# Kernel tuning notes

Hardware: AMD Instinct MI355X
Metric: run time of the kernel (lower is better)

The kernel has to match this reference:

```python
import jax, jax.numpy as jnp
import numpy as np

EMB = 8
HID = 64
B = 1000
T = 512
N = (B * T) // 5  # events per source; sources partition the (batch,time) grid

_KEYS = ["ccba", "cdtx", "cust", "dp", "remit"]
_NUMS = {"ccba": 8, "cdtx": 1, "cust": 1, "dp": 2, "remit": 1}
_CATS = {"ccba": 0, "cdtx": 2, "cust": 3, "dp": 8, "remit": 1}
_VOCAB = {"ccba": 0, "cdtx": 179, "cust": 37, "dp": 435, "remit": 5}


def setup_inputs() -> dict:
    ks = iter(jax.random.split(jax.random.key(0), 64))
    rng = np.random.default_rng(0)
    chunks = np.split(rng.permutation(B * T), 5)
    d = {}
    for k5, ch in zip(_KEYS, chunks):
        d[k5 + "_num"] = jax.random.normal(next(ks), (N, _NUMS[k5]), jnp.float32)
        if _CATS[k5] > 0:
            d[k5 + "_cat"] = jax.random.randint(next(ks), (N, _CATS[k5]), 0, _VOCAB[k5])
            d[k5 + "_tab"] = jax.random.normal(next(ks), (_VOCAB[k5], EMB), jnp.float32) * 0.1
        d[k5 + "_bi"] = jnp.asarray(ch // T, jnp.int32)
        d[k5 + "_ti"] = jnp.asarray(ch % T, jnp.int32)
        in_dim = _CATS[k5] * EMB + _NUMS[k5]
        d[k5 + "_W"] = jax.random.normal(next(ks), (in_dim, HID), jnp.float32) * np.float32(1.0 / np.sqrt(in_dim))
        d[k5 + "_b"] = jnp.zeros((HID,), jnp.float32)
    # LSTM: 2 layers x 2 directions, hidden 64, proj_size 1 -> layer1 input is 2
    for l, insz in [(0, HID), (1, 2)]:
        d[f"Wih{l}"] = jax.random.normal(next(ks), (2, 4 * HID, insz), jnp.float32) * 0.05
        d[f"Whh{l}"] = jax.random.normal(next(ks), (2, 4 * HID, 1), jnp.float32) * 0.05
        d[f"Whr{l}"] = jax.random.normal(next(ks), (2, 1, HID), jnp.float32) * 0.05
        d[f"bih{l}"] = jnp.zeros((2, 4 * HID), jnp.float32)
        d[f"bhh{l}"] = jnp.zeros((2, 4 * HID), jnp.float32)
    d["length"] = T
    d["batch_size"] = B
    return d


def _embed(num, cat, tab, W, b):
    # FeatureEmbedder: concat(categorical embeddings, numeric) -> Linear(hidden)
    x = num if cat is None else jnp.concatenate([tab[cat].reshape(cat.shape[0], -1), num], axis=-1)
    return x @ W + b


def _lstm_dir(x, Wih, Whh, Whr, bih, bhh, reverse):
    Bx = x.shape[0]
    H = Whr.shape[1]
    p = Whr.shape[0]
    bias = bih + bhh

    def step(carry, xt):
        h, c = carry  # h: [B,p] projected hidden, c: [B,H] cell
        g = xt @ Wih.T + h @ Whh.T + bias
        i, f, gg, o = jnp.split(g, 4, axis=-1)  # PyTorch gate order i,f,g,o
        c = jax.nn.sigmoid(f) * c + jax.nn.sigmoid(i) * jnp.tanh(gg)
        h = (jax.nn.sigmoid(o) * jnp.tanh(c)) @ Whr.T  # proj_size projection
        return (h, c), h

    init = (jnp.zeros((Bx, p), x.dtype), jnp.zeros((Bx, H), x.dtype))
    _, ys = jax.lax.scan(step, init, jnp.swapaxes(x, 0, 1), reverse=reverse)
    return jnp.swapaxes(ys, 0, 1)  # [B,T,p]


def _bilstm(x, Wih, Whh, Whr, bih, bhh):
    fwd = _lstm_dir(x, Wih[0], Whh[0], Whr[0], bih[0], bhh[0], False)
    bwd = _lstm_dir(x, Wih[1], Whh[1], Whr[1], bih[1], bhh[1], True)
    return jnp.concatenate([fwd, bwd], axis=-1)


def _forward(a):
    feat = jnp.zeros((a["batch_size"], a["length"], HID), jnp.float32)
    for k5 in _KEYS:
        v = _embed(a[k5 + "_num"], a.get(k5 + "_cat"), a.get(k5 + "_tab"), a[k5 + "_W"], a[k5 + "_b"])
        feat = feat.at[a[k5 + "_bi"], a[k5 + "_ti"]].set(v)  # scatter-assemble padded tensor
    h = _bilstm(feat, a["Wih0"], a["Whh0"], a["Whr0"], a["bih0"], a["bhh0"])
    h = _bilstm(h, a["Wih1"], a["Whh1"], a["Whr1"], a["bih1"], a["bhh1"])
    return h.mean(axis=2)  # [B,T]


def reference(ccba_num, ccba_bi, ccba_ti, ccba_W, ccba_b,
              cdtx_num, cdtx_cat, cdtx_tab, cdtx_bi, cdtx_ti, cdtx_W, cdtx_b,
              cust_num, cust_cat, cust_tab, cust_bi, cust_ti, cust_W, cust_b,
              dp_num, dp_cat, dp_tab, dp_bi, dp_ti, dp_W, dp_b,
              remit_num, remit_cat, remit_tab, remit_bi, remit_ti, remit_W, remit_b,
              Wih0, Whh0, Whr0, bih0, bhh0, Wih1, Whh1, Whr1, bih1, bhh1,
              length, batch_size):
    return _forward(dict(locals()))
```

## Files before the change

### kernel.cpp

```cpp
#include <hip/hip_runtime.h>
#include <cstdint>
#include <cstddef>

#define TLEN 512
#define BATCH 1000
#define NEVS 102400
#define HID 64
#define W0S 16
#define NP (TLEN / W0S)

__device__ __forceinline__ float fast_rcp(float x) {
#if __has_builtin(__builtin_amdgcn_rcpf)
    return __builtin_amdgcn_rcpf(x);
#else
    return 1.0f / x;
#endif
}
__device__ __forceinline__ float sigm(float x) { return fast_rcp(1.0f + __expf(-x)); }
__device__ __forceinline__ float tanh_f(float x) { return fmaf(2.0f, sigm(2.0f * x), -1.0f); }

__device__ __forceinline__ float wave_sum_bcast(float x) {
#if __has_builtin(__builtin_amdgcn_update_dpp) && __has_builtin(__builtin_amdgcn_readlane)
    x += __int_as_float(__builtin_amdgcn_update_dpp(0, __float_as_int(x), 0x111, 0xf, 0xf, true));
    x += __int_as_float(__builtin_amdgcn_update_dpp(0, __float_as_int(x), 0x112, 0xf, 0xf, true));
    x += __int_as_float(__builtin_amdgcn_update_dpp(0, __float_as_int(x), 0x114, 0xf, 0xf, true));
    x += __int_as_float(__builtin_amdgcn_update_dpp(0, __float_as_int(x), 0x118, 0xf, 0xf, true));
    x += __int_as_float(__builtin_amdgcn_update_dpp(0, __float_as_int(x), 0x142, 0xa, 0xf, true));
    x += __int_as_float(__builtin_amdgcn_update_dpp(0, __float_as_int(x), 0x143, 0xc, 0xf, true));
    return __int_as_float(__builtin_amdgcn_readlane(__float_as_int(x), 63));
#else
#pragma unroll
    for (int off = 1; off < 64; off <<= 1) x += __shfl_xor(x, off, 64);
    return x;
#endif
}

__device__ __forceinline__ void wave_sum2(float& a, float& b) {
#if __has_builtin(__builtin_amdgcn_update_dpp) && __has_builtin(__builtin_amdgcn_readlane)
    int ta, tb;
    ta = __builtin_amdgcn_update_dpp(0, __float_as_int(a), 0x111, 0xf, 0xf, true);
    tb = __builtin_amdgcn_update_dpp(0, __float_as_int(b), 0x111, 0xf, 0xf, true);
    a += __int_as_float(ta); b += __int_as_float(tb);
    ta = __builtin_amdgcn_update_dpp(0, __float_as_int(a), 0x112, 0xf, 0xf, true);
    tb = __builtin_amdgcn_update_dpp(0, __float_as_int(b), 0x112, 0xf, 0xf, true);
    a += __int_as_float(ta); b += __int_as_float(tb);
    ta = __builtin_amdgcn_update_dpp(0, __float_as_int(a), 0x114, 0xf, 0xf, true);
    tb = __builtin_amdgcn_update_dpp(0, __float_as_int(b), 0x114, 0xf, 0xf, true);
    a += __int_as_float(ta); b += __int_as_float(tb);
    ta = __builtin_amdgcn_update_dpp(0, __float_as_int(a), 0x118, 0xf, 0xf, true);
    tb = __builtin_amdgcn_update_dpp(0, __float_as_int(b), 0x118, 0xf, 0xf, true);
    a += __int_as_float(ta); b += __int_as_float(tb);
    ta = __builtin_amdgcn_update_dpp(0, __float_as_int(a), 0x142, 0xa, 0xf, true);
    tb = __builtin_amdgcn_update_dpp(0, __float_as_int(b), 0x142, 0xa, 0xf, true);
    a += __int_as_float(ta); b += __int_as_float(tb);
    ta = __builtin_amdgcn_update_dpp(0, __float_as_int(a), 0x143, 0xc, 0xf, true);
    tb = __builtin_amdgcn_update_dpp(0, __float_as_int(b), 0x143, 0xc, 0xf, true);
    a += __int_as_float(ta); b += __int_as_float(tb);
    a = __int_as_float(__builtin_amdgcn_readlane(__float_as_int(a), 63));
    b = __int_as_float(__builtin_amdgcn_readlane(__float_as_int(b), 63));
#else
    a = wave_sum_bcast(a); b = wave_sum_bcast(b);
#endif
}

__global__ __launch_bounds__(256) void map_build_kernel(
    const int* __restrict__ b0, const int* __restrict__ t0,
    const int* __restrict__ b1, const int* __restrict__ t1,
    const int* __restrict__ b2, const int* __restrict__ t2,
    const int* __restrict__ b3, const int* __restrict__ t3,
    const int* __restrict__ b4, const int* __restrict__ t4,
    int* __restrict__ map)
{
    const int src = blockIdx.y;
    const int* bi = src == 0 ? b0 : src == 1 ? b1 : src == 2 ? b2 : src == 3 ? b3 : b4;
    const int* ti = src == 0 ? t0 : src == 1 ? t1 : src == 2 ? t2 : src == 3 ? t3 : t4;
    const int e = blockIdx.x * 256 + threadIdx.x;
    map[bi[e] * TLEN + ti[e]] = (src << 20) | e;
}

__global__ __launch_bounds__(512) void compose_kernel(
    const float* __restrict__ W0, const float* __restrict__ B0,
    const float* __restrict__ W1, const float* __restrict__ B1,
    const float* __restrict__ W2, const float* __restrict__ B2,
    const float* __restrict__ W3, const float* __restrict__ B3,
    const float* __restrict__ W4, const float* __restrict__ B4,
    const float* __restrict__ Wih, const float* __restrict__ bih,
    const float* __restrict__ bhh, float* __restrict__ wp)
{
    const int col = threadIdx.x;
    const int row = blockIdx.x;
    const float* srcW; const float* srcB; int base, IND;
    if (row < 9)        { srcW = W0; srcB = B0; base = 0;   IND = 8;  }
    else if (row < 27)  { srcW = W1; srcB = B1; base = 9;   IND = 17; }
    else if (row < 53)  { srcW = W2; srcB = B2; base = 27;  IND = 25; }
    else if (row < 120) { srcW = W3; srcB = B3; base = 53;  IND = 66; }
    else                { srcW = W4; srcB = B4; base = 120; IND = 9;  }
    const int j = row - base;
    const float* xrow = (j < IND) ? (srcW + (size_t)j * 64) : srcB;
    const float* wr = Wih + (size_t)col * 64;
    float acc = 0.0f;
#pragma unroll
    for (int h2 = 0; h2 < 64; ++h2) acc = fmaf(xrow[h2], wr[h2], acc);
    if (j == IND) acc += bih[col] + bhh[col];
    wp[(size_t)row * 512 + col] = acc;
}

template<bool HI>
__device__ __forceinline__ void fused_path(
    const float* __restrict__ wp, const int* __restrict__ map,
    const float* __restrict__ ccba_num,
    const float* __restrict__ cdtx_num, const int* __restrict__ cdtx_cat, const float* __restrict__ cdtx_tab,
    const float* __restrict__ cust_num, const int* __restrict__ cust_cat, const float* __restrict__ cust_tab,
    const float* __restrict__ dp_num,   const int* __restrict__ dp_cat,   const float* __restrict__ dp_tab,
    const float* __restrict__ remit_num, const int* __restrict__ remit_cat, const float* __restrict__ remit_tab,
    const float* __restrict__ Whh, const float* __restrict__ Whr,
    float* __restrict__ h0, int b, int dir, int tid,
    float (&winP)[2][W0S][256], float (&xbuf)[2][W0S][68], int (&mcls)[2][W0S])
{
    constexpr int C0 = HI ? 3 : 5,  O0 = HI ? 5 : 0;
    constexpr int C1 = HI ? 8 : 9,  O1 = HI ? 9 : 0;
    constexpr int C2 = HI ? 12 : 13, O2 = HI ? 13 : 0;
    constexpr int C3 = HI ? 32 : 34, O3 = HI ? 34 : 0;
    constexpr int C4 = HI ? 4 : 5,  O4 = HI ? 5 : 0;

    const int pcol = tid & 255;
    const int col = dir * 256 + pcol;

    float w0[C0], w1[C1], w2[C2], w3[C3], w4[C4];
#pragma unroll
    for (int j = 0; j < C0; ++j) w0[j] = wp[(size_t)(0 + O0 + j) * 512 + col];
#pragma unroll
    for (int j = 0; j < C1; ++j) w1[j] = wp[(size_t)(9 + O1 + j) * 512 + col];
#pragma unroll
    for (int j = 0; j < C2; ++j) w2[j] = wp[(size_t)(27 + O2 + j) * 512 + col];
#pragma unroll
    for (int j = 0; j < C3; ++j) w3[j] = wp[(size_t)(53 + O3 + j) * 512 + col];
#pragma unroll
    for (int j = 0; j < C4; ++j) w4[j] = wp[(size_t)(120 + O4 + j) * 512 + col];
    float bias0 = 0, bias1 = 0, bias2 = 0, bias3 = 0, bias4 = 0;
    if (HI) {
        bias0 = wp[(size_t)8 * 512 + col];
        bias1 = wp[(size_t)26 * 512 + col];
        bias2 = wp[(size_t)52 * 512 + col];
        bias3 = wp[(size_t)119 * 512 + col];
        bias4 = wp[(size_t)129 * 512 + col];
    }

    const int lane = tid & 63;
    float whh4[4] = {0, 0, 0, 0};
    float whr = 0.0f, h = 0.0f, c = 0.0f;
    if (!HI && tid < 64) {
#pragma unroll
        for (int k = 0; k < 4; ++k) whh4[k] = Whh[dir * 256 + k * 64 + lane];
        whr = Whr[dir * HID + lane];
    }
    float* h0p = h0 + (size_t)b * TLEN * 2 + dir;

    auto dot_evt = [&](int mc, const float* xb) -> float {
        const int src = mc >> 20;
        float a0 = 0.f, a1 = 0.f, bb = 0.f;
        switch (src) {
        case 0:
#pragma unroll
            for (int j = 0; j < C0; ++j) {
                if (j & 1) a1 = fmaf(xb[O0 + j], w0[j], a1); else a0 = fmaf(xb[O0 + j], w0[j], a0);
            }
            bb = bias0; break;
        case 1:
#pragma unroll
            for (int j = 0; j < C1; ++j) {
                if (j & 1) a1 = fmaf(xb[O1 + j], w1[j], a1); else a0 = fmaf(xb[O1 + j], w1[j], a0);
            }
            bb = bias1; break;
        case 2:
#pragma unroll
            for (int j = 0; j < C2; ++j) {
                if (j & 1) a1 = fmaf(xb[O2 + j], w2[j], a1); else a0 = fmaf(xb[O2 + j], w2[j], a0);
            }
            bb = bias2; break;
        case 3:
#pragma unroll
            for (int j = 0; j < C3; ++j) {
                if (j & 1) a1 = fmaf(xb[O3 + j], w3[j], a1); else a0 = fmaf(xb[O3 + j], w3[j], a0);
            }
            bb = bias3; break;
        default:
#pragma unroll
            for (int j = 0; j < C4; ++j) {
                if (j & 1) a1 = fmaf(xb[O4 + j], w4[j], a1); else a0 = fmaf(xb[O4 + j], w4[j], a0);
            }
            bb = bias4; break;
        }
        return HI ? (bb + a0 + a1) : (a0 + a1);
    };

    auto gather_phase = [&](int P, int slot) {
        const int ev = tid >> 5, v = tid & 31;
        const int s = P * W0S + ev;
        const int t = dir ? (TLEN - 1 - s) : s;
        const int mc = map[b * TLEN + t];
        if (v == 0) mcls[slot][ev] = mc;
        const int src = mc >> 20, e = mc & 0xFFFFF;
        switch (src) {
        case 0:
            if (v < 8) xbuf[slot][ev][v] = ccba_num[(size_t)e * 8 + v];
            break;
        case 1:
            if (v < 17) xbuf[slot][ev][v] = (v < 16)
                ? cdtx_tab[(size_t)cdtx_cat[e * 2 + (v >> 3)] * 8 + (v & 7)] : cdtx_num[e];
            break;
        case 2:
            if (v < 25) xbuf[slot][ev][v] = (v < 24)
                ? cust_tab[(size_t)cust_cat[e * 3 + (v >> 3)] * 8 + (v & 7)] : cust_num[e];
            break;
        case 3:
#pragma unroll
            for (int vv = v; vv < 66; vv += 32)
                xbuf[slot][ev][vv] = (vv < 64)
                    ? dp_tab[(size_t)dp_cat[e * 8 + (vv >> 3)] * 8 + (vv & 7)]
                    : dp_num[(size_t)e * 2 + (vv - 64)];
            break;
        default:
            if (v < 9) xbuf[slot][ev][v] = (v < 8)
                ? remit_tab[(size_t)remit_cat[e] * 8 + v] : remit_num[e];
            break;
        }
    };

    auto dots_phase = [&](int slot) {
#pragma unroll 1
        for (int sl = 0; sl < W0S; sl += 2) {
            const int mc0 = mcls[slot][sl];
            const int mc1 = mcls[slot][sl + 1];
            const float a = dot_evt(mc0, xbuf[slot][sl]);
            const float bq = dot_evt(mc1, xbuf[slot][sl + 1]);
            winP[HI ? 1 : 0][sl][pcol] = a;
            winP[HI ? 1 : 0][sl + 1][pcol] = bq;
        }
    };

    gather_phase(0, 0);
    __syncthreads();

    for (int p = 0; p < NP; ++p) {
        if (p + 1 < NP) gather_phase(p + 1, (p + 1) & 1);
        dots_phase(p & 1);
        __syncthreads();

        if (!HI && tid < 64) {
            float G0[4], G1[4];
#pragma unroll
            for (int k = 0; k < 4; ++k) {
                G0[k] = winP[0][0][k * 64 + lane];
                G1[k] = winP[1][0][k * 64 + lane];
            }
            for (int sl = 0; sl < W0S; ++sl) {
                const int sn = (sl + 1 < W0S) ? sl + 1 : sl;
                float N0[4], N1[4];
#pragma unroll
                for (int k = 0; k < 4; ++k) {
                    N0[k] = winP[0][sn][k * 64 + lane];
                    N1[k] = winP[1][sn][k * 64 + lane];
                }
                const float gi = fmaf(whh4[0], h, G0[0] + G1[0]);
                const float gf = fmaf(whh4[1], h, G0[1] + G1[1]);
                const float gg = fmaf(whh4[2], h, G0[2] + G1[2]);
                const float go = fmaf(whh4[3], h, G0[3] + G1[3]);
                c = sigm(gf) * c + sigm(gi) * tanh_f(gg);
                h = wave_sum_bcast(sigm(go) * tanh_f(c) * whr);
                const int s = p * W0S + sl;
                const int t = dir ? (TLEN - 1 - s) : s;
                if (lane == 0) h0p[(size_t)t * 2] = h;
#pragma unroll
                for (int k = 0; k < 4; ++k) { G0[k] = N0[k]; G1[k] = N1[k]; }
            }
        }
        __syncthreads();
    }
}

__global__ __launch_bounds__(512, 4) void fused0_kernel(
    const float* __restrict__ ccba_num,
    const float* __restrict__ cdtx_num, const int* __restrict__ cdtx_cat, const float* __restrict__ cdtx_tab,
    const float* __restrict__ cust_num, const int* __restrict__ cust_cat, const float* __restrict__ cust_tab,
    const float* __restrict__ dp_num,   const int* __restrict__ dp_cat,   const float* __restrict__ dp_tab,
    const float* __restrict__ remit_num, const int* __restrict__ remit_cat, const float* __restrict__ remit_tab,
    const float* __restrict__ wp, const int* __restrict__ map,
    const float* __restrict__ Whh, const float* __restrict__ Whr,
    float* __restrict__ h0)
{
    __shared__ float winP[2][W0S][256];
    __shared__ float xbuf[2][W0S][68];
    __shared__ int   mcls[2][W0S];
    const int tid = threadIdx.x;
    const int b = blockIdx.x >> 1, dir = blockIdx.x & 1;
    if (tid < 256)
        fused_path<false>(wp, map, ccba_num,
            cdtx_num, cdtx_cat, cdtx_tab, cust_num, cust_cat, cust_tab,
            dp_num, dp_cat, dp_tab, remit_num, remit_cat, remit_tab,
            Whh, Whr, h0, b, dir, tid, winP, xbuf, mcls);
    else
        fused_path<true>(wp, map, ccba_num,
            cdtx_num, cdtx_cat, cdtx_tab, cust_num, cust_cat, cust_tab,
            dp_num, dp_cat, dp_tab, remit_num, remit_cat, remit_tab,
            Whh, Whr, h0, b, dir, tid, winP, xbuf, mcls);
}

__global__ __launch_bounds__(256) void lstm1_kernel(
    const float* __restrict__ h0, const float* __restrict__ Wih,
    const float* __restrict__ Whh, const float* __restrict__ Whr,
    const float* __restrict__ bih, const float* __restrict__ bhh,
    float* __restrict__ h1)
{
    const int w = threadIdx.x >> 6, lane = threadIdx.x & 63;
    const int b = blockIdx.x * 4 + w;

    float wi0[2][4], wi1[2][4], whh[2][4], bias[2][4], whr[2];
#pragma unroll
    for (int d = 0; d < 2; ++d) {
#pragma unroll
        for (int k = 0; k < 4; ++k) {
            const int r = d * 256 + k * 64 + lane;
            wi0[d][k] = Wih[(size_t)r * 2 + 0];
            wi1[d][k] = Wih[(size_t)r * 2 + 1];
            whh[d][k] = Whh[r];
            bias[d][k] = bih[r] + bhh[r];
        }
        whr[d] = Whr[d * HID + lane];
    }
    float hA = 0, cA = 0, hB = 0, cB = 0;
    const float* hb = h0 + (size_t)b * TLEN * 2;

    float2 xA = *(const float2*)(hb);
    float2 xB = *(const float2*)(hb + (size_t)(TLEN - 1) * 2);
    for (int t = 0; t < TLEN; ++t) {
        const int tn = (t + 1 < TLEN) ? t + 1 : t;
        const float2 xAn = *(const float2*)(hb + (size_t)tn * 2);
        const float2 xBn = *(const float2*)(hb + (size_t)(TLEN - 1 - tn) * 2);
        float gA[4], gB[4];
#pragma unroll
        for (int k = 0; k < 4; ++k) {
            gA[k] = fmaf(whh[0][k], hA, fmaf(wi1[0][k], xA.y, fmaf(wi0[0][k], xA.x, bias[0][k])));
            gB[k] = fmaf(whh[1][k], hB, fmaf(wi1[1][k], xB.y, fmaf(wi0[1][k], xB.x, bias[1][k])));
        }
        cA = sigm(gA[1]) * cA + sigm(gA[0]) * tanh_f(gA[2]);
        cB = sigm(gB[1]) * cB + sigm(gB[0]) * tanh_f(gB[2]);
        float pA = sigm(gA[3]) * tanh_f(cA) * whr[0];
        float pB = sigm(gB[3]) * tanh_f(cB) * whr[1];
        wave_sum2(pA, pB);
        hA = pA; hB = pB;
        if (lane == 0) {
            h1[((size_t)b * TLEN + t) * 2 + 0] = hA;
            h1[((size_t)b * TLEN + (TLEN - 1 - t)) * 2 + 1] = hB;
        }
        xA = xAn; xB = xBn;
    }
}

__global__ __launch_bounds__(256) void mean_kernel(
    const float2* __restrict__ h1, float* __restrict__ out)
{
    int i = blockIdx.x * 256 + threadIdx.x;
    if (i < BATCH * TLEN) {
        float2 v = h1[i];
        out[i] = 0.5f * (v.x + v.y);
    }
}

extern "C" void kernel_launch(void* const* d_in, const int* in_sizes, int n_in,
                              void* d_out, int out_size, void* d_ws, size_t ws_size,
                              hipStream_t stream)
{
    const float* ccba_num = (const float*)d_in[0];
    const int*   ccba_bi  = (const int*)d_in[1];
    const int*   ccba_ti  = (const int*)d_in[2];
    const float* ccba_W   = (const float*)d_in[3];
    const float* ccba_b   = (const float*)d_in[4];
    const float* cdtx_num = (const float*)d_in[5];
    const int*   cdtx_cat = (const int*)d_in[6];
    const float* cdtx_tab = (const float*)d_in[7];
    const int*   cdtx_bi  = (const int*)d_in[8];
    const int*   cdtx_ti  = (const int*)d_in[9];
    const float* cdtx_W   = (const float*)d_in[10];
    const float* cdtx_b   = (const float*)d_in[11];
    const float* cust_num = (const float*)d_in[12];
    const int*   cust_cat = (const int*)d_in[13];
    const float* cust_tab = (const float*)d_in[14];
    const int*   cust_bi  = (const int*)d_in[15];
    const int*   cust_ti  = (const int*)d_in[16];
    const float* cust_W   = (const float*)d_in[17];
    const float* cust_b   = (const float*)d_in[18];
    const float* dp_num   = (const float*)d_in[19];
    const int*   dp_cat   = (const int*)d_in[20];
    const float* dp_tab   = (const float*)d_in[21];
    const int*   dp_bi    = (const int*)d_in[22];
    const int*   dp_ti    = (const int*)d_in[23];
    const float* dp_W     = (const float*)d_in[24];
    const float* dp_b     = (const float*)d_in[25];
    const float* remit_num = (const float*)d_in[26];
    const int*   remit_cat = (const int*)d_in[27];
    const float* remit_tab = (const float*)d_in[28];
    const int*   remit_bi  = (const int*)d_in[29];
    const int*   remit_ti  = (const int*)d_in[30];
    const float* remit_W   = (const float*)d_in[31];
    const float* remit_b   = (const float*)d_in[32];
    const float* Wih0 = (const float*)d_in[33];
    const float* Whh0 = (const float*)d_in[34];
    const float* Whr0 = (const float*)d_in[35];
    const float* bih0 = (const float*)d_in[36];
    const float* bhh0 = (const float*)d_in[37];
    const float* Wih1 = (const float*)d_in[38];
    const float* Whh1 = (const float*)d_in[39];
    const float* Whr1 = (const float*)d_in[40];
    const float* bih1 = (const float*)d_in[41];
    const float* bhh1 = (const float*)d_in[42];

    float* out = (float*)d_out;

    char* ws = (char*)d_ws;
    float* wp  = (float*)ws;
    int*   map = (int*)  (ws + 266240ull);
    float* h0  = (float*)(ws + 266240ull + 2048000ull);
    float* h1  = (float*)(ws + 266240ull + 2048000ull + 4096000ull);

    compose_kernel<<<130, 512, 0, stream>>>(
        ccba_W, ccba_b, cdtx_W, cdtx_b, cust_W, cust_b,
        dp_W, dp_b, remit_W, remit_b, Wih0, bih0, bhh0, wp);

    map_build_kernel<<<dim3(NEVS / 256, 5), 256, 0, stream>>>(
        ccba_bi, ccba_ti, cdtx_bi, cdtx_ti, cust_bi, cust_ti,
        dp_bi, dp_ti, remit_bi, remit_ti, map);

    fused0_kernel<<<2 * BATCH, 512, 0, stream>>>(
        ccba_num,
        cdtx_num, cdtx_cat, cdtx_tab,
        cust_num, cust_cat, cust_tab,
        dp_num, dp_cat, dp_tab,
        remit_num, remit_cat, remit_tab,
        wp, map, Whh0, Whr0, h0);

    lstm1_kernel<<<250, 256, 0, stream>>>(h0, Wih1, Whh1, Whr1, bih1, bhh1, h1);
    mean_kernel<<<(BATCH * TLEN + 255) / 256, 256, 0, stream>>>((const float2*)h1, out);
}
```

Before: 1.478 ms.

## Restructure fused layer-0 kernel with LDS weights and a dedicated recurrence wave

Each block copies its direction's composed input-projection weights (132x256 floats) into shared memory. Every thread computes four gate columns per event with float4 dot products, using a bias-one trick in the padded inputs so no separate bias add is needed. A separate 64-thread wave runs the sequential LSTM recurrence while the other 512 threads gather and project the next window, in a three-stage software pipeline with a smaller window of 8. The change also bumps lstm1 launch bounds and reads its weights through volatile pointers. The aim is to take the projection off the recurrence's critical path, at the cost of about 135KB of LDS, one block per CU, and a barrier every 8 steps.

```diff
diff --git a/kernel.cpp b/kernel.cpp
--- a/kernel.cpp
+++ b/kernel.cpp
@@ -6,7 +6,7 @@
 #define BATCH 1000
 #define NEVS 102400
 #define HID 64
-#define W0S 16
+#define W0S 8
 #define NP (TLEN / W0S)
 
 __device__ __forceinline__ float fast_rcp(float x) {
@@ -105,181 +105,30 @@
     wp[(size_t)row * 512 + col] = acc;
 }
 
-template<bool HI>
-__device__ __forceinline__ void fused_path(
-    const float* __restrict__ wp, const int* __restrict__ map,
-    const float* __restrict__ ccba_num,
-    const float* __restrict__ cdtx_num, const int* __restrict__ cdtx_cat, const float* __restrict__ cdtx_tab,
-    const float* __restrict__ cust_num, const int* __restrict__ cust_cat, const float* __restrict__ cust_tab,
-    const float* __restrict__ dp_num,   const int* __restrict__ dp_cat,   const float* __restrict__ dp_tab,
-    const float* __restrict__ remit_num, const int* __restrict__ remit_cat, const float* __restrict__ remit_tab,
-    const float* __restrict__ Whh, const float* __restrict__ Whr,
-    float* __restrict__ h0, int b, int dir, int tid,
-    float (&winP)[2][W0S][256], float (&xbuf)[2][W0S][68], int (&mcls)[2][W0S])
-{
-    constexpr int C0 = HI ? 3 : 5,  O0 = HI ? 5 : 0;
-    constexpr int C1 = HI ? 8 : 9,  O1 = HI ? 9 : 0;
-    constexpr int C2 = HI ? 12 : 13, O2 = HI ? 13 : 0;
-    constexpr int C3 = HI ? 32 : 34, O3 = HI ? 34 : 0;
-    constexpr int C4 = HI ? 4 : 5,  O4 = HI ? 5 : 0;
-
-    const int pcol = tid & 255;
-    const int col = dir * 256 + pcol;
-
-    float w0[C0], w1[C1], w2[C2], w3[C3], w4[C4];
-#pragma unroll
-    for (int j = 0; j < C0; ++j) w0[j] = wp[(size_t)(0 + O0 + j) * 512 + col];
-#pragma unroll
-    for (int j = 0; j < C1; ++j) w1[j] = wp[(size_t)(9 + O1 + j) * 512 + col];
-#pragma unroll
-    for (int j = 0; j < C2; ++j) w2[j] = wp[(size_t)(27 + O2 + j) * 512 + col];
-#pragma unroll
-    for (int j = 0; j < C3; ++j) w3[j] = wp[(size_t)(53 + O3 + j) * 512 + col];
-#pragma unroll
-    for (int j = 0; j < C4; ++j) w4[j] = wp[(size_t)(120 + O4 + j) * 512 + col];
-    float bias0 = 0, bias1 = 0, bias2 = 0, bias3 = 0, bias4 = 0;
-    if (HI) {
-        bias0 = wp[(size_t)8 * 512 + col];
-        bias1 = wp[(size_t)26 * 512 + col];
-        bias2 = wp[(size_t)52 * 512 + col];
-        bias3 = wp[(size_t)119 * 512 + col];
-        bias4 = wp[(size_t)129 * 512 + col];
-    }
-
-    const int lane = tid & 63;
-    float whh4[4] = {0, 0, 0, 0};
-    float whr = 0.0f, h = 0.0f, c = 0.0f;
-    if (!HI && tid < 64) {
-#pragma unroll
-        for (int k = 0; k < 4; ++k) whh4[k] = Whh[dir * 256 + k * 64 + lane];
-        whr = Whr[dir * HID + lane];
-    }
-    float* h0p = h0 + (size_t)b * TLEN * 2 + dir;
-
-    auto dot_evt = [&](int mc, const float* xb) -> float {
-        const int src = mc >> 20;
-        float a0 = 0.f, a1 = 0.f, bb = 0.f;
-        switch (src) {
-        case 0:
-#pragma unroll
-            for (int j = 0; j < C0; ++j) {
-                if (j & 1) a1 = fmaf(xb[O0 + j], w0[j], a1); else a0 = fmaf(xb[O0 + j], w0[j], a0);
-            }
-            bb = bias0; break;
-        case 1:
-#pragma unroll
-            for (int j = 0; j < C1; ++j) {
-                if (j & 1) a1 = fmaf(xb[O1 + j], w1[j], a1); else a0 = fmaf(xb[O1 + j], w1[j], a0);
-            }
-            bb = bias1; break;
-        case 2:
-#pragma unroll
-            for (int j = 0; j < C2; ++j) {
-                if (j & 1) a1 = fmaf(xb[O2 + j], w2[j], a1); else a0 = fmaf(xb[O2 + j], w2[j], a0);
-            }
-            bb = bias2; break;
-        case 3:
-#pragma unroll
-            for (int j = 0; j < C3; ++j) {
-                if (j & 1) a1 = fmaf(xb[O3 + j], w3[j], a1); else a0 = fmaf(xb[O3 + j], w3[j], a0);
-            }
-            bb = bias3; break;
-        default:
-#pragma unroll
-            for (int j = 0; j < C4; ++j) {
-                if (j & 1) a1 = fmaf(xb[O4 + j], w4[j], a1); else a0 = fmaf(xb[O4 + j], w4[j], a0);
-            }
-            bb = bias4; break;
-        }
-        return HI ? (bb + a0 + a1) : (a0 + a1);
-    };
-
-    auto gather_phase = [&](int P, int slot) {
-        const int ev = tid >> 5, v = tid & 31;
-        const int s = P * W0S + ev;
-        const int t = dir ? (TLEN - 1 - s) : s;
-        const int mc = map[b * TLEN + t];
-        if (v == 0) mcls[slot][ev] = mc;
-        const int src = mc >> 20, e = mc & 0xFFFFF;
-        switch (src) {
-        case 0:
-            if (v < 8) xbuf[slot][ev][v] = ccba_num[(size_t)e * 8 + v];
-            break;
-        case 1:
-            if (v < 17) xbuf[slot][ev][v] = (v < 16)
-                ? cdtx_tab[(size_t)cdtx_cat[e * 2 + (v >> 3)] * 8 + (v & 7)] : cdtx_num[e];
-            break;
-        case 2:
-            if (v < 25) xbuf[slot][ev][v] = (v < 24)
-                ? cust_tab[(size_t)cust_cat[e * 3 + (v >> 3)] * 8 + (v & 7)] : cust_num[e];
-            break;
-        case 3:
-#pragma unroll
-            for (int vv = v; vv < 66; vv += 32)
-                xbuf[slot][ev][vv] = (vv < 64)
-                    ? dp_tab[(size_t)dp_cat[e * 8 + (vv >> 3)] * 8 + (vv & 7)]
-                    : dp_num[(size_t)e * 2 + (vv - 64)];
-            break;
-        default:
-            if (v < 9) xbuf[slot][ev][v] = (v < 8)
-                ? remit_tab[(size_t)remit_cat[e] * 8 + v] : remit_num[e];
-            break;
-        }
-    };
-
-    auto dots_phase = [&](int slot) {
-#pragma unroll 1
-        for (int sl = 0; sl < W0S; sl += 2) {
-            const int mc0 = mcls[slot][sl];
-            const int mc1 = mcls[slot][sl + 1];
-            const float a = dot_evt(mc0, xbuf[slot][sl]);
-            const float bq = dot_evt(mc1, xbuf[slot][sl + 1]);
-            winP[HI ? 1 : 0][sl][pcol] = a;
-            winP[HI ? 1 : 0][sl + 1][pcol] = bq;
-        }
-    };
-
-    gather_phase(0, 0);
-    __syncthreads();
-
-    for (int p = 0; p < NP; ++p) {
-        if (p + 1 < NP) gather_phase(p + 1, (p + 1) & 1);
-        dots_phase(p & 1);
-        __syncthreads();
-
-        if (!HI && tid < 64) {
-            float G0[4], G1[4];
-#pragma unroll
-            for (int k = 0; k < 4; ++k) {
-                G0[k] = winP[0][0][k * 64 + lane];
-                G1[k] = winP[1][0][k * 64 + lane];
-            }
-            for (int sl = 0; sl < W0S; ++sl) {
-                const int sn = (sl + 1 < W0S) ? sl + 1 : sl;
-                float N0[4], N1[4];
-#pragma unroll
-                for (int k = 0; k < 4; ++k) {
-                    N0[k] = winP[0][sn][k * 64 + lane];
-                    N1[k] = winP[1][sn][k * 64 + lane];
-                }
-                const float gi = fmaf(whh4[0], h, G0[0] + G1[0]);
-                const float gf = fmaf(whh4[1], h, G0[1] + G1[1]);
-                const float gg = fmaf(whh4[2], h, G0[2] + G1[2]);
-                const float go = fmaf(whh4[3], h, G0[3] + G1[3]);
-                c = sigm(gf) * c + sigm(gi) * tanh_f(gg);
-                h = wave_sum_bcast(sigm(go) * tanh_f(c) * whr);
-                const int s = p * W0S + sl;
-                const int t = dir ? (TLEN - 1 - s) : s;
-                if (lane == 0) h0p[(size_t)t * 2] = h;
-#pragma unroll
-                for (int k = 0; k < 4; ++k) { G0[k] = N0[k]; G1[k] = N1[k]; }
-            }
-        }
-        __syncthreads();
-    }
-}
-
-__global__ __launch_bounds__(512, 4) void fused0_kernel(
+template<int NB, int BASE>
+__device__ __forceinline__ float4 dot4(const float* wT, const float* xb, int colq) {
+    float ax = 0.f, ay = 0.f, az = 0.f, aw = 0.f;
+#pragma unroll
+    for (int jb = 0; jb < NB; ++jb) {
+        const float4 x4 = *(const float4*)(xb + 4 * jb);
+        const float* w = wT + (size_t)(BASE + 4 * jb) * 256 + 4 * colq;
+        const float4 w0 = *(const float4*)(w);
+        const float4 w1 = *(const float4*)(w + 256);
+        const float4 w2 = *(const float4*)(w + 512);
+        const float4 w3 = *(const float4*)(w + 768);
+        ax = fmaf(x4.x, w0.x, ax); ay = fmaf(x4.x, w0.y, ay);
+        az = fmaf(x4.x, w0.z, az); aw = fmaf(x4.x, w0.w, aw);
+        ax = fmaf(x4.y, w1.x, ax); ay = fmaf(x4.y, w1.y, ay);
+        az = fmaf(x4.y, w1.z, az); aw = fmaf(x4.y, w1.w, aw);
+        ax = fmaf(x4.z, w2.x, ax); ay = fmaf(x4.z, w2.y, ay);
+        az = fmaf(x4.z, w2.z, az); aw = fmaf(x4.z, w2.w, aw);
+        ax = fmaf(x4.w, w3.x, ax); ay = fmaf(x4.w, w3.y, ay);
+        az = fmaf(x4.w, w3.z, az); aw = fmaf(x4.w, w3.w, aw);
+    }
+    return make_float4(ax, ay, az, aw);
+}
+
+__global__ __launch_bounds__(576, 1) void fused0_kernel(
     const float* __restrict__ ccba_num,
     const float* __restrict__ cdtx_num, const int* __restrict__ cdtx_cat, const float* __restrict__ cdtx_tab,
     const float* __restrict__ cust_num, const int* __restrict__ cust_cat, const float* __restrict__ cust_tab,
@@ -289,24 +138,129 @@
     const float* __restrict__ Whh, const float* __restrict__ Whr,
     float* __restrict__ h0)
 {
+    __shared__ float wT[132 * 256];
     __shared__ float winP[2][W0S][256];
     __shared__ float xbuf[2][W0S][68];
     __shared__ int   mcls[2][W0S];
+
     const int tid = threadIdx.x;
     const int b = blockIdx.x >> 1, dir = blockIdx.x & 1;
-    if (tid < 256)
-        fused_path<false>(wp, map, ccba_num,
-            cdtx_num, cdtx_cat, cdtx_tab, cust_num, cust_cat, cust_tab,
-            dp_num, dp_cat, dp_tab, remit_num, remit_cat, remit_tab,
-            Whh, Whr, h0, b, dir, tid, winP, xbuf, mcls);
-    else
-        fused_path<true>(wp, map, ccba_num,
-            cdtx_num, cdtx_cat, cdtx_tab, cust_num, cust_cat, cust_tab,
-            dp_num, dp_cat, dp_tab, remit_num, remit_cat, remit_tab,
-            Whh, Whr, h0, b, dir, tid, winP, xbuf, mcls);
-}
-
-__global__ __launch_bounds__(256) void lstm1_kernel(
+
+    {
+        const float4* wp4 = (const float4*)wp;
+        float4* wT4 = (float4*)wT;
+        for (int i = tid; i < 130 * 64; i += 576) {
+            const int row = i >> 6, c4 = i & 63;
+            wT4[(row << 6) + c4] = wp4[(row << 7) + (dir << 6) + c4];
+        }
+        if (tid < 128) wT4[130 * 64 + tid] = make_float4(0.f, 0.f, 0.f, 0.f);
+    }
+
+    float whh4[4] = {0.f, 0.f, 0.f, 0.f};
+    float whr = 0.f, h = 0.f, c = 0.f;
+    float* h0p = h0 + (size_t)b * TLEN * 2 + dir;
+    if (tid >= 512) {
+        const int lane = tid - 512;
+#pragma unroll
+        for (int k = 0; k < 4; ++k) whh4[k] = Whh[dir * 256 + k * 64 + lane];
+        whr = Whr[dir * HID + lane];
+    }
+
+    struct GR { float v0, v1; int mc; };
+
+    auto g_load = [&](int P) -> GR {
+        GR g; g.v0 = 0.f; g.v1 = 0.f;
+        const int ev = tid >> 6, v = tid & 63;
+        const int s = P * W0S + ev;
+        const int t = dir ? (TLEN - 1 - s) : s;
+        g.mc = map[b * TLEN + t];
+        const int src = g.mc >> 20, e = g.mc & 0xFFFFF;
+        switch (src) {
+        case 0:
+            g.v0 = (v < 8) ? ccba_num[(size_t)e * 8 + v] : (v == 8 ? 1.0f : 0.0f);
+            break;
+        case 1:
+            g.v0 = (v < 16) ? cdtx_tab[(size_t)cdtx_cat[e * 2 + (v >> 3)] * 8 + (v & 7)]
+                 : (v == 16 ? cdtx_num[e] : (v == 17 ? 1.0f : 0.0f));
+            break;
+        case 2:
+            g.v0 = (v < 24) ? cust_tab[(size_t)cust_cat[e * 3 + (v >> 3)] * 8 + (v & 7)]
+                 : (v == 24 ? cust_num[e] : (v == 25 ? 1.0f : 0.0f));
+            break;
+        case 3:
+            g.v0 = dp_tab[(size_t)dp_cat[e * 8 + (v >> 3)] * 8 + (v & 7)];
+            if (v < 4) g.v1 = (v < 2) ? dp_num[(size_t)e * 2 + v] : (v == 2 ? 1.0f : 0.0f);
+            break;
+        default:
+            g.v0 = (v < 8) ? remit_tab[(size_t)remit_cat[e] * 8 + v]
+                 : (v == 8 ? remit_num[e] : (v == 9 ? 1.0f : 0.0f));
+            break;
+        }
+        return g;
+    };
+    auto g_store = [&](const GR& g, int P) {
+        const int buf = P & 1;
+        const int ev = tid >> 6, v = tid & 63;
+        if (v == 0) mcls[buf][ev] = g.mc;
+        const int src = g.mc >> 20;
+        const int pad = (src == 0) ? 12 : (src == 1) ? 20 : (src == 2) ? 28
+                      : (src == 3) ? 64 : 12;
+        if (v < pad) xbuf[buf][ev][v] = g.v0;
+        if (src == 3 && v < 4) xbuf[buf][ev][64 + v] = g.v1;
+    };
+
+    auto a1 = [&](int P) {
+        const int buf = P & 1;
+        const int ev = tid >> 6, colq = tid & 63;
+        const int src = mcls[buf][ev] >> 20;
+        const float* xb = xbuf[buf][ev];
+        float4 acc;
+        switch (src) {
+        case 0:  acc = dot4<3, 0>(wT, xb, colq);   break;
+        case 1:  acc = dot4<5, 9>(wT, xb, colq);   break;
+        case 2:  acc = dot4<7, 27>(wT, xb, colq);  break;
+        case 3:  acc = dot4<17, 53>(wT, xb, colq); break;
+        default: acc = dot4<3, 120>(wT, xb, colq); break;
+        }
+        ((float4*)winP[buf][ev])[colq] = acc;
+    };
+
+    auto bstep = [&](int P) {
+        const int buf = P & 1;
+        const int lane = tid - 512;
+        for (int sl = 0; sl < W0S; ++sl) {
+            const float gi = fmaf(whh4[0], h, winP[buf][sl][lane]);
+            const float gf = fmaf(whh4[1], h, winP[buf][sl][64 + lane]);
+            const float gg = fmaf(whh4[2], h, winP[buf][sl][128 + lane]);
+            const float go = fmaf(whh4[3], h, winP[buf][sl][192 + lane]);
+            c = sigm(gf) * c + sigm(gi) * tanh_f(gg);
+            h = wave_sum_bcast(sigm(go) * tanh_f(c) * whr);
+            const int s = P * W0S + sl;
+            const int tt = dir ? (TLEN - 1 - s) : s;
+            if (lane == 0) h0p[(size_t)tt * 2] = h;
+        }
+    };
+
+    if (tid < 512) { GR g0 = g_load(0); g_store(g0, 0); }
+    __syncthreads();
+    if (tid < 512) { GR g1 = g_load(1); a1(0); g_store(g1, 1); }
+    __syncthreads();
+
+    for (int p = 0; p < NP; ++p) {
+        if (tid < 512) {
+            GR g{};
+            const bool hg = (p + 2 < NP);
+            if (hg) g = g_load(p + 2);
+            if (p + 1 < NP) a1(p + 1);
+            if (hg) g_store(g, p + 2);
+        } else if (tid < 576) {
+            bstep(p);
+        }
+        __syncthreads();
+    }
+}
+
+__global__ __launch_bounds__(256, 2) void lstm1_kernel(
     const float* __restrict__ h0, const float* __restrict__ Wih,
     const float* __restrict__ Whh, const float* __restrict__ Whr,
     const float* __restrict__ bih, const float* __restrict__ bhh,
@@ -315,18 +269,24 @@
     const int w = threadIdx.x >> 6, lane = threadIdx.x & 63;
     const int b = blockIdx.x * 4 + w;
 
+    const volatile float* vWih = Wih;
+    const volatile float* vWhh = Whh;
+    const volatile float* vWhr = Whr;
+    const volatile float* vbih = bih;
+    const volatile float* vbhh = bhh;
+
     float wi0[2][4], wi1[2][4], whh[2][4], bias[2][4], whr[2];
 #pragma unroll
     for (int d = 0; d < 2; ++d) {
 #pragma unroll
         for (int k = 0; k < 4; ++k) {
             const int r = d * 256 + k * 64 + lane;
-            wi0[d][k] = Wih[(size_t)r * 2 + 0];
-            wi1[d][k] = Wih[(size_t)r * 2 + 1];
-            whh[d][k] = Whh[r];
-            bias[d][k] = bih[r] + bhh[r];
-        }
-        whr[d] = Whr[d * HID + lane];
+            wi0[d][k] = vWih[(size_t)r * 2 + 0];
+            wi1[d][k] = vWih[(size_t)r * 2 + 1];
+            whh[d][k] = vWhh[r];
+            bias[d][k] = vbih[r] + vbhh[r];
+        }
+        whr[d] = vWhr[d * HID + lane];
     }
     float hA = 0, cA = 0, hB = 0, cB = 0;
     const float* hb = h0 + (size_t)b * TLEN * 2;
@@ -431,7 +391,7 @@
         ccba_bi, ccba_ti, cdtx_bi, cdtx_ti, cust_bi, cust_ti,
         dp_bi, dp_ti, remit_bi, remit_ti, map);
 
-    fused0_kernel<<<2 * BATCH, 512, 0, stream>>>(
+    fused0_kernel<<<2 * BATCH, 576, 0, stream>>>(
         ccba_num,
         cdtx_num, cdtx_cat, cdtx_tab,
         cust_num, cust_cat, cust_tab,
```

Result: no change. 1.459 ms (-1.3%).
